# Optimization experiments

Measured on AMD Instinct MI355X. Metric: run time of the kernel, lower is better.

The kernel has to match this reference:

```python
import jax, jax.numpy as jnp
import numpy as np

N_NODES = 50000
N_EDGES = 800000
IN_DIM = 256
OUT_DIM = 128


def setup_inputs() -> dict:
    key = jax.random.key(0)
    k1, k2, k3, k4, k5 = jax.random.split(key, 5)
    adj_rows = jax.random.randint(k1, (N_EDGES,), 0, N_NODES, dtype=jnp.int32)
    adj_cols = jax.random.randint(k2, (N_EDGES,), 0, N_NODES, dtype=jnp.int32)
    adj_vals = jax.random.uniform(k3, (N_EDGES,), dtype=jnp.float32)
    x = jax.random.normal(k4, (N_NODES, IN_DIM), dtype=jnp.float32)
    # kaiming_normal-ish init for weight
    W = jax.random.normal(k5, (IN_DIM, OUT_DIM), dtype=jnp.float32) * np.sqrt(2.0 / IN_DIM)
    b = jnp.zeros((OUT_DIM,), dtype=jnp.float32)
    return {"adj_rows": adj_rows, "adj_cols": adj_cols, "adj_vals": adj_vals,
            "x": x, "W": W, "b": b}


def reference(adj_rows, adj_cols, adj_vals, x, W, b):
    # support = X @ W  (dense GEMM)
    support = x @ W  # [N, OUT_DIM]
    # sparse A @ support via edge-parallel gather + segment-sum (COO SpMM)
    msgs = adj_vals[:, None] * support[adj_cols]  # [E, OUT_DIM]
    out = jax.ops.segment_sum(msgs, adj_rows, num_segments=x.shape[0])
    return out + b
```

## Files before the change

### kernel.cpp

```cpp
#include <hip/hip_runtime.h>
#include <hip/hip_bf16.h>

#define N_NODES 50000
#define N_EDGES 800000
#define IN_DIM  256
#define OUT_DIM 128

#define NBINS        512
#define ROWS_PER_BIN 98
#define HALF_ROWS    49
#define BIN_CAP      1920
#define EPB          2048
#define NB_BIN       391
#define NB_GEMM      391
#define CUR_STRIDE   32

typedef __bf16 bf16x8 __attribute__((ext_vector_type(8)));
typedef float  f32x4  __attribute__((ext_vector_type(4)));

__device__ __forceinline__ unsigned bin_of(unsigned r) { return (r * 85599u) >> 23; }
__device__ __forceinline__ float blo(unsigned u) { return __uint_as_float(u << 16); }
__device__ __forceinline__ float bhi(unsigned u) { return __uint_as_float(u & 0xffff0000u); }

#define WF_OFF   0
#define SUP_OFF  65536
#define BIN_OFF  12865536
#define CUR_OFF  20729856

__global__ void k_prep(const float* __restrict__ W, __bf16* __restrict__ Wf,
                       int* __restrict__ bin_cursor) {
    int t = blockIdx.x * 256 + threadIdx.x;
    if (t < 32768) {
        int s = t >> 3, j = t & 7;
        int nrow = ((s >> 9) << 4) | (s & 15);
        int k    = (((s >> 4) & 3) << 3) | (((s >> 6) & 7) << 5) | j;
        Wf[t] = (__bf16)W[k * OUT_DIM + nrow];
    }
    if (t < NBINS) bin_cursor[t * CUR_STRIDE] = t * BIN_CAP;
}

__global__ __launch_bounds__(512, 4) void k_fuse(const float* __restrict__ x,
                                                 const __bf16* __restrict__ Wf,
                                                 unsigned* __restrict__ sup32,
                                                 const int* __restrict__ rows,
                                                 const int* __restrict__ cols,
                                                 const float* __restrict__ vals,
                                                 int* __restrict__ bin_cursor,
                                                 int2* __restrict__ binbuf) {
    __shared__ union {
        uint4 sB[4096];
        struct { int cur[NBINS]; int base[NBINS]; } bin;
    } sh;
    int t = threadIdx.x;

    if (blockIdx.x < NB_GEMM) {
        const uint4* wf4 = (const uint4*)Wf;
#pragma unroll
        for (int r = 0; r < 8; ++r) sh.sB[r * 512 + t] = wf4[r * 512 + t];
        __syncthreads();

        int  wave = t >> 6;
        int  lane = t & 63;
        long tile = (long)blockIdx.x * 8 + wave;
        if (tile >= 3125) return;
        int  m    = lane & 15;
        int  quad = lane >> 4;

        const float* aprow = x + (tile * 16 + m) * IN_DIM + quad * 8;

        float4 fa[16];
#pragma unroll
        for (int ks = 0; ks < 8; ++ks) {
            fa[2 * ks]     = *(const float4*)(aprow + ks * 32);
            fa[2 * ks + 1] = *(const float4*)(aprow + ks * 32 + 4);
        }
        bf16x8 ab[8];
#pragma unroll
        for (int ks = 0; ks < 8; ++ks) {
            float4 f0 = fa[2 * ks];
            float4 f1 = fa[2 * ks + 1];
            ab[ks] = (bf16x8){(__bf16)f0.x, (__bf16)f0.y, (__bf16)f0.z, (__bf16)f0.w,
                              (__bf16)f1.x, (__bf16)f1.y, (__bf16)f1.z, (__bf16)f1.w};
        }

        f32x4 acc[8];
#pragma unroll
        for (int n = 0; n < 8; ++n) acc[n] = (f32x4){0, 0, 0, 0};

        const __bf16* sbh = (const __bf16*)sh.sB;
#pragma unroll
        for (int ks = 0; ks < 8; ++ks) {
#pragma unroll
            for (int n = 0; n < 8; ++n) {
                bf16x8 bfr = *(const bf16x8*)(sbh + (((n * 8 + ks) * 64 + lane) << 3));
                acc[n] = __builtin_amdgcn_mfma_f32_16x16x32_bf16(ab[ks], bfr, acc[n], 0, 0, 0);
            }
        }

        unsigned* op = sup32 + (long)tile * 16 * 64;
#pragma unroll
        for (int r = 0; r < 4; ++r) {
#pragma unroll
            for (int n = 0; n < 4; ++n) {
                __bf16 lo = (__bf16)acc[n][r], hi = (__bf16)acc[n + 4][r];
                unsigned w = (unsigned)*(unsigned short*)&lo |
                             ((unsigned)*(unsigned short*)&hi << 16);
                op[(quad * 4 + r) * 64 + n * 16 + m] = w;
            }
        }
    } else {
        long e0 = (long)(blockIdx.x - NB_GEMM) * EPB;
        sh.bin.cur[t] = 0;
        __syncthreads();

        int2 rec[4];
        int  lrank[4];
        bool full = (e0 + EPB <= N_EDGES);

        if (full) {
#pragma unroll
            for (int k = 0; k < 4; ++k) {
                long e = e0 + k * 512 + t;
                unsigned r = (unsigned)rows[e];
                unsigned c = (unsigned)cols[e];
                float    w = vals[e];
                rec[k]   = make_int2((int)((r << 16) | c), __float_as_int(w));
                lrank[k] = atomicAdd(&sh.bin.cur[bin_of(r)], 1);
            }
        } else {
#pragma unroll
            for (int k = 0; k < 4; ++k) {
                long e = e0 + k * 512 + t;
                lrank[k] = -1;
                if (e < N_EDGES) {
                    unsigned r = (unsigned)rows[e];
                    unsigned c = (unsigned)cols[e];
                    float    w = vals[e];
                    rec[k]   = make_int2((int)((r << 16) | c), __float_as_int(w));
                    lrank[k] = atomicAdd(&sh.bin.cur[bin_of(r)], 1);
                }
            }
        }
        __syncthreads();

        sh.bin.base[t] = atomicAdd(&bin_cursor[t * CUR_STRIDE], sh.bin.cur[t]);
        __syncthreads();

#pragma unroll
        for (int k = 0; k < 4; ++k) {
            if (lrank[k] >= 0) {
                unsigned bn = bin_of(((unsigned)rec[k].x) >> 16);
                int dst = sh.bin.base[bn] + lrank[k];
                if (dst < (int)(bn + 1) * BIN_CAP)
                    binbuf[dst] = rec[k];
            }
        }
    }
}

__global__ __launch_bounds__(512, 4) void k_sg(const int* __restrict__ bin_cursor,
                                               const int2* __restrict__ binbuf,
                                               const unsigned* __restrict__ sup,
                                               const float* __restrict__ bias,
                                               float* __restrict__ out) {
    __shared__ int2 sorted_[BIN_CAP];
    __shared__ unsigned gbuf[8][16][64];
    __shared__ int  cnt[64], off[64], cur[64], s[64];
    int blk = blockIdx.x, t = threadIdx.x;
    int bin  = blk >> 1;
    int row0 = bin * ROWS_PER_BIN + (blk & 1) * HALF_ROWS;

    int n = bin_cursor[bin * CUR_STRIDE] - bin * BIN_CAP;
    n = n < 0 ? 0 : (n > BIN_CAP ? BIN_CAP : n);
    const int2* seg = binbuf + (long)bin * BIN_CAP;

    if (t < 64) cnt[t] = 0;
    __syncthreads();

    for (int i = t; i < n; i += 512) {
        int rl = (int)(((unsigned)seg[i].x) >> 16) - row0;
        if ((unsigned)rl < HALF_ROWS) atomicAdd(&cnt[rl], 1);
    }
    __syncthreads();

    int v = 0;
    if (t < 64) { v = cnt[t]; s[t] = v; }
    __syncthreads();
#pragma unroll
    for (int o = 1; o < 64; o <<= 1) {
        int xv = 0;
        if (t < 64 && t >= o) xv = s[t - o];
        __syncthreads();
        if (t < 64) s[t] += xv;
        __syncthreads();
    }
    if (t < 64) { off[t] = s[t] - v; cur[t] = 0; }
    __syncthreads();

    for (int i = t; i < n; i += 512) {
        int2 rec = seg[i];
        int rl = (int)(((unsigned)rec.x) >> 16) - row0;
        if ((unsigned)rl < HALF_ROWS)
            sorted_[off[rl] + atomicAdd(&cur[rl], 1)] = rec;
    }
    __syncthreads();

    int wave = t >> 6, lane = t & 63;
    float bb0 = bias[lane], bb1 = bias[64 + lane];
    unsigned* gb = &gbuf[wave][0][0];

    for (int rl = wave; rl < HALF_ROWS; rl += 8) {
        int row = row0 + rl;
        if (row >= N_NODES) continue;
        int st = off[rl], nd = cnt[rl];
        float a0 = 0.f, a1 = 0.f;
        for (int i = 0; i < nd; i += 16) {
            float vv[16];
#pragma unroll
            for (int j = 0; j < 16; ++j) {
                int ok = (i + j) < nd;
                int2 rec = sorted_[ok ? st + i + j : st];
                vv[j] = ok ? __int_as_float(rec.y) : 0.f;
                const unsigned* gp = sup + (long)(rec.x & 0xffff) * 64 + lane;
                __builtin_amdgcn_global_load_lds(
                    (const __attribute__((address_space(1))) unsigned*)gp,
                    (__attribute__((address_space(3))) unsigned*)(gb + j * 64),
                    4, 0, 0);
            }
            asm volatile("s_waitcnt vmcnt(0)" ::: "memory");
#pragma unroll
            for (int j = 0; j < 16; ++j) {
                unsigned u = gb[j * 64 + lane];
                a0 += vv[j] * blo(u);
                a1 += vv[j] * bhi(u);
            }
        }
        out[(long)row * 128 + lane]      = a0 + bb0;
        out[(long)row * 128 + 64 + lane] = a1 + bb1;
    }
}

extern "C" void kernel_launch(void* const* d_in, const int* in_sizes, int n_in,
                              void* d_out, int out_size, void* d_ws, size_t ws_size,
                              hipStream_t stream) {
    const int*   adj_rows = (const int*)  d_in[0];
    const int*   adj_cols = (const int*)  d_in[1];
    const float* adj_vals = (const float*)d_in[2];
    const float* x        = (const float*)d_in[3];
    const float* W        = (const float*)d_in[4];
    const float* b        = (const float*)d_in[5];
    float* out = (float*)d_out;

    char* ws = (char*)d_ws;
    __bf16*   Wf         = (__bf16*)  (ws + WF_OFF);
    unsigned* sup32      = (unsigned*)(ws + SUP_OFF);
    int2*     binbuf     = (int2*)    (ws + BIN_OFF);
    int*      bin_cursor = (int*)     (ws + CUR_OFF);

    k_prep<<<128, 256, 0, stream>>>(W, Wf, bin_cursor);
    k_fuse<<<NB_GEMM + NB_BIN, 512, 0, stream>>>(x, Wf, sup32,
                                                 adj_rows, adj_cols, adj_vals,
                                                 bin_cursor, binbuf);
    k_sg  <<<NBINS * 2, 512, 0, stream>>>(bin_cursor, binbuf, sup32, b, out);
}
```

Measured before the change: 167.2 us.

## Gather support rows into registers, process two rows per wave, remap block order

The gather phase of k_sg now loads bf16 support rows straight into registers instead of staging them in LDS through global_load_lds. Each wave now handles two output rows at once, interleaving their 8-deep gathers to keep more independent loads in flight. The 32KB LDS staging buffer is gone, which may raise occupancy. Block-to-bin mapping is also permuted so that concurrent blocks spread across bins. The cost is more registers per thread and wasted loads whenever the paired rows have uneven degrees.

```diff
diff --git a/kernel.cpp b/kernel.cpp
--- a/kernel.cpp
+++ b/kernel.cpp
@@ -164,11 +164,11 @@
                                                const float* __restrict__ bias,
                                                float* __restrict__ out) {
     __shared__ int2 sorted_[BIN_CAP];
-    __shared__ unsigned gbuf[8][16][64];
     __shared__ int  cnt[64], off[64], cur[64], s[64];
     int blk = blockIdx.x, t = threadIdx.x;
-    int bin  = blk >> 1;
-    int row0 = bin * ROWS_PER_BIN + (blk & 1) * HALF_ROWS;
+    int bin  = (blk & 7) * 64 + (blk >> 4);
+    int half = (blk >> 3) & 1;
+    int row0 = bin * ROWS_PER_BIN + half * HALF_ROWS;
 
     int n = bin_cursor[bin * CUR_STRIDE] - bin * BIN_CAP;
     n = n < 0 ? 0 : (n > BIN_CAP ? BIN_CAP : n);
@@ -207,36 +207,48 @@
 
     int wave = t >> 6, lane = t & 63;
     float bb0 = bias[lane], bb1 = bias[64 + lane];
-    unsigned* gb = &gbuf[wave][0][0];
-
-    for (int rl = wave; rl < HALF_ROWS; rl += 8) {
-        int row = row0 + rl;
-        if (row >= N_NODES) continue;
-        int st = off[rl], nd = cnt[rl];
-        float a0 = 0.f, a1 = 0.f;
-        for (int i = 0; i < nd; i += 16) {
-            float vv[16];
-#pragma unroll
-            for (int j = 0; j < 16; ++j) {
-                int ok = (i + j) < nd;
-                int2 rec = sorted_[ok ? st + i + j : st];
-                vv[j] = ok ? __int_as_float(rec.y) : 0.f;
-                const unsigned* gp = sup + (long)(rec.x & 0xffff) * 64 + lane;
-                __builtin_amdgcn_global_load_lds(
-                    (const __attribute__((address_space(1))) unsigned*)gp,
-                    (__attribute__((address_space(3))) unsigned*)(gb + j * 64),
-                    4, 0, 0);
-            }
-            asm volatile("s_waitcnt vmcnt(0)" ::: "memory");
-#pragma unroll
-            for (int j = 0; j < 16; ++j) {
-                unsigned u = gb[j * 64 + lane];
-                a0 += vv[j] * blo(u);
-                a1 += vv[j] * bhi(u);
-            }
-        }
-        out[(long)row * 128 + lane]      = a0 + bb0;
-        out[(long)row * 128 + 64 + lane] = a1 + bb1;
+
+    for (int p = 0; p < 4; ++p) {
+        int rlA = wave + p * 16;
+        int rlB = rlA + 8;
+        bool hasA = (rlA < HALF_ROWS) && (row0 + rlA < N_NODES);
+        bool hasB = (rlB < HALF_ROWS) && (row0 + rlB < N_NODES);
+        if (!hasA && !hasB) continue;
+        int stA = 0, ndA = 0, stB = 0, ndB = 0;
+        if (hasA) { stA = off[rlA]; ndA = cnt[rlA]; }
+        if (hasB) { stB = off[rlB]; ndB = cnt[rlB]; }
+        float a0A = 0.f, a1A = 0.f, a0B = 0.f, a1B = 0.f;
+
+        int rounds = ndA > ndB ? ndA : ndB;
+        for (int i = 0; i < rounds; i += 8) {
+            unsigned uA[8], uB[8]; float vA[8], vB[8];
+#pragma unroll
+            for (int j = 0; j < 8; ++j) {
+                int okA = (i + j) < ndA;
+                int2 rA = sorted_[okA ? stA + i + j : stA];
+                vA[j] = okA ? __int_as_float(rA.y) : 0.f;
+                uA[j] = sup[(long)(((unsigned)rA.x) & 0xffffu) * 64 + lane];
+                int okB = (i + j) < ndB;
+                int2 rB = sorted_[okB ? stB + i + j : stB];
+                vB[j] = okB ? __int_as_float(rB.y) : 0.f;
+                uB[j] = sup[(long)(((unsigned)rB.x) & 0xffffu) * 64 + lane];
+            }
+#pragma unroll
+            for (int j = 0; j < 8; ++j) {
+                a0A += vA[j] * blo(uA[j]); a1A += vA[j] * bhi(uA[j]);
+                a0B += vB[j] * blo(uB[j]); a1B += vB[j] * bhi(uB[j]);
+            }
+        }
+        if (hasA) {
+            int row = row0 + rlA;
+            out[(long)row * 128 + lane]      = a0A + bb0;
+            out[(long)row * 128 + 64 + lane] = a1A + bb1;
+        }
+        if (hasB) {
+            int row = row0 + rlB;
+            out[(long)row * 128 + lane]      = a0B + bb0;
+            out[(long)row * 128 + 64 + lane] = a1B + bb1;
+        }
     }
 }
 
```

Result: faster. 160.5 us (-4.0%).

## Gather support rows with 16-byte vector loads across four edges per wave

Applied to the files above, without the earlier changes.

Replaces the per-lane 4-byte global-to-LDS gathers and LDS staging buffer with direct 16-byte register loads. Each 16-lane group now reads one full support row for a different edge, so a wave handles four edges per load instruction. Partial sums are combined across the groups with xor shuffles, and one group writes the result as float4 stores. This cuts load instruction count and LDS traffic and frees shared memory, at the cost of more accumulator registers and a shuffle reduction per row.

```diff
diff --git a/kernel.cpp b/kernel.cpp
--- a/kernel.cpp
+++ b/kernel.cpp
@@ -164,7 +164,6 @@
                                                const float* __restrict__ bias,
                                                float* __restrict__ out) {
     __shared__ int2 sorted_[BIN_CAP];
-    __shared__ unsigned gbuf[8][16][64];
     __shared__ int  cnt[64], off[64], cur[64], s[64];
     int blk = blockIdx.x, t = threadIdx.x;
     int bin  = blk >> 1;
@@ -206,37 +205,54 @@
     __syncthreads();
 
     int wave = t >> 6, lane = t & 63;
-    float bb0 = bias[lane], bb1 = bias[64 + lane];
-    unsigned* gb = &gbuf[wave][0][0];
+    int g = lane >> 4;
+    int k = lane & 15;
+    float4 bbLo = ((const float4*)bias)[k];
+    float4 bbHi = ((const float4*)bias)[k + 16];
 
     for (int rl = wave; rl < HALF_ROWS; rl += 8) {
         int row = row0 + rl;
         if (row >= N_NODES) continue;
         int st = off[rl], nd = cnt[rl];
-        float a0 = 0.f, a1 = 0.f;
+        float aL0 = 0.f, aL1 = 0.f, aL2 = 0.f, aL3 = 0.f;
+        float aH0 = 0.f, aH1 = 0.f, aH2 = 0.f, aH3 = 0.f;
+
         for (int i = 0; i < nd; i += 16) {
-            float vv[16];
-#pragma unroll
-            for (int j = 0; j < 16; ++j) {
-                int ok = (i + j) < nd;
-                int2 rec = sorted_[ok ? st + i + j : st];
+            uint4 u[4]; float vv[4];
+#pragma unroll
+            for (int j = 0; j < 4; ++j) {
+                int e  = i + 4 * j + g;
+                int ok = e < nd;
+                int2 rec = sorted_[ok ? st + e : st];
                 vv[j] = ok ? __int_as_float(rec.y) : 0.f;
-                const unsigned* gp = sup + (long)(rec.x & 0xffff) * 64 + lane;
-                __builtin_amdgcn_global_load_lds(
-                    (const __attribute__((address_space(1))) unsigned*)gp,
-                    (__attribute__((address_space(3))) unsigned*)(gb + j * 64),
-                    4, 0, 0);
-            }
-            asm volatile("s_waitcnt vmcnt(0)" ::: "memory");
-#pragma unroll
-            for (int j = 0; j < 16; ++j) {
-                unsigned u = gb[j * 64 + lane];
-                a0 += vv[j] * blo(u);
-                a1 += vv[j] * bhi(u);
-            }
-        }
-        out[(long)row * 128 + lane]      = a0 + bb0;
-        out[(long)row * 128 + 64 + lane] = a1 + bb1;
+                u[j]  = *(const uint4*)(sup + (long)(((unsigned)rec.x) & 0xffffu) * 64 + k * 4);
+            }
+#pragma unroll
+            for (int j = 0; j < 4; ++j) {
+                aL0 += vv[j] * blo(u[j].x); aH0 += vv[j] * bhi(u[j].x);
+                aL1 += vv[j] * blo(u[j].y); aH1 += vv[j] * bhi(u[j].y);
+                aL2 += vv[j] * blo(u[j].z); aH2 += vv[j] * bhi(u[j].z);
+                aL3 += vv[j] * blo(u[j].w); aH3 += vv[j] * bhi(u[j].w);
+            }
+        }
+
+#pragma unroll
+        for (int mask = 16; mask < 64; mask <<= 1) {
+            aL0 += __shfl_xor(aL0, mask, 64);
+            aL1 += __shfl_xor(aL1, mask, 64);
+            aL2 += __shfl_xor(aL2, mask, 64);
+            aL3 += __shfl_xor(aL3, mask, 64);
+            aH0 += __shfl_xor(aH0, mask, 64);
+            aH1 += __shfl_xor(aH1, mask, 64);
+            aH2 += __shfl_xor(aH2, mask, 64);
+            aH3 += __shfl_xor(aH3, mask, 64);
+        }
+        if (g == 0) {
+            float4 oLo = {aL0 + bbLo.x, aL1 + bbLo.y, aL2 + bbLo.z, aL3 + bbLo.w};
+            float4 oHi = {aH0 + bbHi.x, aH1 + bbHi.y, aH2 + bbHi.z, aH3 + bbHi.w};
+            *(float4*)(out + (long)row * 128 + 4 * k)      = oLo;
+            *(float4*)(out + (long)row * 128 + 64 + 4 * k) = oHi;
+        }
     }
 }
 
```

Measured after the change: 150.2 us. 10.2% less time.
